# Performance work log

Measured on AMD Instinct MI355X. Metric: run time of the kernel, lower is better.

The kernel has to match this reference:

```python
import jax, jax.numpy as jnp
import numpy as np

N = 50000
E = 1280000
D = 64          # in_features = hidden_size = out_features
HEADS = 1
NEG_SLOPE = 0.2
EPS_COS = 1e-8
EPS_SM = 1e-16


def _xavier(key, shape):
    fan_in, fan_out = shape[0], shape[-1]
    lim = float(np.sqrt(6.0 / (fan_in + fan_out)))
    return jax.random.uniform(key, shape, jnp.float32, -lim, lim)


def setup_inputs() -> dict:
    key = jax.random.key(0)
    ks = jax.random.split(key, 16)
    x = jax.random.normal(ks[0], (N, D), jnp.float32)
    edge_index = jax.random.randint(ks[1], (2, E), 0, N, jnp.int64)
    edge_attr = jax.random.uniform(ks[2], (E,), jnp.float32)
    return {
        "x": x,
        "edge_index": edge_index,
        "edge_attr": edge_attr,
        # COSGAT layer 0 (in D -> out D, heads=1)
        "W0": _xavier(ks[3], (D, HEADS * D)),
        "att0": _xavier(ks[4], (HEADS, 2 * D)),
        "beta0": jnp.zeros((HEADS,), jnp.float32),
        "b0": jnp.zeros((HEADS * D,), jnp.float32),
        # COSGAT layer 1
        "W1": _xavier(ks[5], (D, HEADS * D)),
        "att1": _xavier(ks[6], (HEADS, 2 * D)),
        "beta1": jnp.zeros((HEADS,), jnp.float32),
        "b1": jnp.zeros((HEADS * D,), jnp.float32),
        # LinearEncoder residual branch
        "rW1": _xavier(ks[7], (D, D)),
        "rb1": jnp.zeros((D,), jnp.float32),
        "rW2": _xavier(ks[8], (D, D)),
        "rb2": jnp.zeros((D,), jnp.float32),
    }


def _seg_softmax(logits, idx, n):
    # softmax over edges grouped by target node idx; logits [E, H]
    m = jax.ops.segment_max(logits, idx, num_segments=n)
    ex = jnp.exp(logits - m[idx])
    s = jax.ops.segment_sum(ex, idx, num_segments=n)
    return ex / (s[idx] + EPS_SM)


def _cosgat(x, src, dst, w, W, att, beta, bias):
    n = x.shape[0]
    H = (x @ W).reshape(n, HEADS, -1)           # [N, H, C]
    Hi, Hj = H[dst], H[src]                      # [E, H, C]
    # GAT logits: att . [Hi || Hj]
    logits = (jnp.einsum('ehc,hc->eh', Hi, att[:, :H.shape[-1]])
              + jnp.einsum('ehc,hc->eh', Hj, att[:, H.shape[-1]:]))
    logits = jnp.where(logits >= 0, logits, NEG_SLOPE * logits)
    # cosine similarity on original features
    xi, xj = x[dst], x[src]
    ni = jnp.maximum(jnp.linalg.norm(xi, axis=-1), EPS_COS)
    nj = jnp.maximum(jnp.linalg.norm(xj, axis=-1), EPS_COS)
    cos = jnp.sum(xi * xj, axis=-1) / (ni * nj)  # [E]
    cos = jnp.broadcast_to(cos[:, None], logits.shape)
    gat_alpha = _seg_softmax(logits, dst, n)
    cos_alpha = _seg_softmax(cos, dst, n)
    b = jax.nn.sigmoid(beta)[None, :]            # [1, H]
    fused = (1.0 - b) * gat_alpha + b * cos_alpha
    w_cl = jnp.minimum(w, 4.0)
    gate = jnp.clip(1.0 - w_cl / 4.0, 0.0, 1.0)[:, None]  # [E, 1]
    final = _seg_softmax(fused * gate, dst, n)   # [E, H]
    msg = Hj * final[:, :, None]                 # [E, H, C]
    out = jax.ops.segment_sum(msg, dst, num_segments=n)
    out = out.reshape(n, -1) + bias              # concat heads + bias
    return jax.nn.elu(out)


def reference(x, edge_index, edge_attr, W0, att0, beta0, b0,
              W1, att1, beta1, b1, rW1, rb1, rW2, rb2):
    src, dst = edge_index[0], edge_index[1]      # PyG: i = target = edge_index[1]
    # residual MLP: Linear -> relu -> Linear (dropout p=0, eval)
    x_res = jax.nn.relu(x @ rW1 + rb1) @ rW2 + rb2
    h = _cosgat(x, src, dst, edge_attr, W0, att0, beta0, b0)
    h = jax.nn.elu(h)                            # inter-layer elu in encoder
    h = _cosgat(h, src, dst, edge_attr, W1, att1, beta1, b1)
    return h + x_res
```

## Files before the change

kernel.cpp:

```cpp
#include <hip/hip_runtime.h>
#include <hip/hip_bf16.h>
#include <math.h>


constexpr int D = 64;
constexpr int CAP = 64;
constexpr float NEG_SLOPE = 0.2f;
constexpr float EPS_COS = 1e-8f;
constexpr float EPS_SM = 1e-16f;

#if defined(__has_builtin)
#if __has_builtin(__builtin_amdgcn_cvt_pk_f32_fp8) && __has_builtin(__builtin_amdgcn_cvt_pk_fp8_f32)
#define HW_FP8 1
#endif
#endif

typedef float floatx2 __attribute__((ext_vector_type(2)));

__device__ __forceinline__ float wred_sum(float v) {
#pragma unroll
  for (int off = 32; off > 0; off >>= 1) v += __shfl_xor(v, off, 64);
  return v;
}
__device__ __forceinline__ float wred_max(float v) {
#pragma unroll
  for (int off = 32; off > 0; off >>= 1) v = fmaxf(v, __shfl_xor(v, off, 64));
  return v;
}
__device__ __forceinline__ float elu1(float x) { return x > 0.f ? x : __expf(x) - 1.f; }
__device__ __forceinline__ float sane(float v) {
  return (v == v && fabsf(v) < 1e30f) ? v : 0.f;
}
__device__ __forceinline__ float ldv(const void* p, size_t i, int f32) {
  return f32 ? ((const float*)p)[i]
             : __bfloat162float(((const __hip_bfloat16*)p)[i]);
}
__device__ __forceinline__ void stv(void* p, size_t i, int f32, float v) {
  if (f32) ((float*)p)[i] = v;
  else ((__hip_bfloat16*)p)[i] = __float2bfloat16(v);
}
__device__ __forceinline__ float b2f(unsigned short u) {
  return __uint_as_float(((unsigned int)u) << 16);
}
__device__ __forceinline__ void unp8(uint4 u, float* f) {
  f[0] = __uint_as_float(u.x << 16);
  f[1] = __uint_as_float(u.x & 0xffff0000u);
  f[2] = __uint_as_float(u.y << 16);
  f[3] = __uint_as_float(u.y & 0xffff0000u);
  f[4] = __uint_as_float(u.z << 16);
  f[5] = __uint_as_float(u.z & 0xffff0000u);
  f[6] = __uint_as_float(u.w << 16);
  f[7] = __uint_as_float(u.w & 0xffff0000u);
}

__device__ __forceinline__ unsigned char enc_fp8(float v) {
#ifdef HW_FP8
  int pk = __builtin_amdgcn_cvt_pk_fp8_f32(v, v, 0, false);
  return (unsigned char)(pk & 0xFF);
#else
  _Float16 h = (_Float16)v;
  unsigned short ub;
  __builtin_memcpy(&ub, &h, 2);
  return (unsigned char)((ub + 0x80) >> 8);
#endif
}
__device__ __forceinline__ void dec_fp8x8(uint2 u, float* f) {
#ifdef HW_FP8
  floatx2 a = __builtin_amdgcn_cvt_pk_f32_fp8(u.x, false);
  floatx2 b = __builtin_amdgcn_cvt_pk_f32_fp8(u.x, true);
  floatx2 c = __builtin_amdgcn_cvt_pk_f32_fp8(u.y, false);
  floatx2 d = __builtin_amdgcn_cvt_pk_f32_fp8(u.y, true);
  f[0] = a[0]; f[1] = a[1]; f[2] = b[0]; f[3] = b[1];
  f[4] = c[0]; f[5] = c[1]; f[6] = d[0]; f[7] = d[1];
#else
#pragma unroll
  for (int i = 0; i < 8; ++i) {
    unsigned int byte = (i < 4 ? (u.x >> (8 * i)) : (u.y >> (8 * (i - 4)))) & 0xFF;
    unsigned short hb = (unsigned short)(byte << 8);
    _Float16 h;
    __builtin_memcpy(&h, &hb, 2);
    f[i] = (float)h;
  }
#endif
}

__device__ __forceinline__ unsigned int pack_sg(int src, float g) {
  int gq = (int)(g * 16383.f + 0.5f);
  return ((unsigned int)src & 0x3FFFFu) | ((unsigned int)gq << 18);
}
__device__ __forceinline__ int upk_src(unsigned int e, int N) {
  return min((int)(e & 0x3FFFFu), N - 1);
}
__device__ __forceinline__ float upk_gate(unsigned int e) {
  return (float)(e >> 18) * (1.f / 16383.f);
}
__device__ __forceinline__ float gate_of(float w) {
  return fminf(fmaxf(1.f - 0.25f * fminf(w, 4.f), 0.f), 1.f);
}

__device__ float slow_cos(const unsigned char* __restrict__ fhat, int a, int b) {
  const uint2* fa = (const uint2*)(fhat + (size_t)a * D);
  const uint2* fb = (const uint2*)(fhat + (size_t)b * D);
  float dsum = 0.f;
  for (int q = 0; q < 8; ++q) {
    float va[8], vb[8];
    dec_fp8x8(fa[q], va);
    dec_fp8x8(fb[q], vb);
#pragma unroll
    for (int i = 0; i < 8; ++i) dsum += va[i] * vb[i];
  }
  return dsum;
}

__device__ __forceinline__ void prep_node(float f, int f32, int wid, int lane,
                                          const void* __restrict__ W,
                                          const void* __restrict__ att,
                                          unsigned char* __restrict__ fhat,
                                          __hip_bfloat16* __restrict__ Hmat,
                                          float* __restrict__ a_l,
                                          float* __restrict__ a_r,
                                          float* __restrict__ ls) {
  float n2 = wred_sum(f * f);
  float nrm = fmaxf(sqrtf(n2), EPS_COS);
  fhat[(size_t)wid * D + lane] = enc_fp8(f / nrm);
  ls[lane] = f;
  __syncthreads();
  float h0 = 0.f, h1 = 0.f, h2 = 0.f, h3 = 0.f;
  if (f32) {
    const float* Wf = (const float*)W;
#pragma unroll 4
    for (int k = 0; k < D; k += 4) {
      h0 += ls[k] * Wf[k * D + lane];
      h1 += ls[k + 1] * Wf[(k + 1) * D + lane];
      h2 += ls[k + 2] * Wf[(k + 2) * D + lane];
      h3 += ls[k + 3] * Wf[(k + 3) * D + lane];
    }
  } else {
    const __hip_bfloat16* Wb = (const __hip_bfloat16*)W;
#pragma unroll 4
    for (int k = 0; k < D; k += 4) {
      h0 += ls[k] * __bfloat162float(Wb[k * D + lane]);
      h1 += ls[k + 1] * __bfloat162float(Wb[(k + 1) * D + lane]);
      h2 += ls[k + 2] * __bfloat162float(Wb[(k + 2) * D + lane]);
      h3 += ls[k + 3] * __bfloat162float(Wb[(k + 3) * D + lane]);
    }
  }
  float Hc = (h0 + h1) + (h2 + h3);
  Hmat[(size_t)wid * D + lane] = __float2bfloat16(Hc);
  float al = wred_sum(Hc * ldv(att, lane, f32));
  float ar = wred_sum(Hc * ldv(att, D + lane, f32));
  if (lane == 0) {
    a_l[wid] = al;
    a_r[wid] = ar;
  }
  __syncthreads();
}

__global__ void __launch_bounds__(64) k_all(const unsigned short* __restrict__ xu,
                                            const int* __restrict__ ei,
                                            const void* __restrict__ w,
                                            int* __restrict__ flags,
                                            int* __restrict__ cnt,
                                            const void* __restrict__ x,
                                            const void* __restrict__ W,
                                            const void* __restrict__ att,
                                            unsigned char* __restrict__ fhat,
                                            __hip_bfloat16* __restrict__ Hmat,
                                            float* __restrict__ a_l,
                                            float* __restrict__ a_r,
                                            unsigned int* __restrict__ csr2,
                                            int N, int E) {
  __shared__ float ls[D];
  const int lane = threadIdx.x;
  const int b = blockIdx.x;
  float dv = b2f(xu[lane]);
  float da = fabsf(dv);
  unsigned long long m = __ballot(da > 1e-4f && da < 100.f);
  unsigned long long m2 = __ballot(ei[2 * lane + 1] != 0);
  const int f32 = (__popcll(m) >= 60) ? 0 : 1;
  const int wide = (m2 == 0ull) ? 1 : 0;
  if (b == 0 && lane == 0) {
    flags[0] = f32;
    flags[1] = wide;
  }
  const long long e0 = ((long long)b * E) / N;
  const long long e1 = ((long long)(b + 1) * E) / N;
  for (long long e = e0 + lane; e < e1; e += 64) {
    int ss, dd;
    if (wide) {
      ss = ei[2 * e];
      dd = ei[2 * (size_t)E + 2 * e];
    } else {
      ss = ei[e];
      dd = ei[(size_t)E + e];
    }
    float we = ldv(w, (size_t)e, f32);
    const int dc = min(max(dd, 0), N - 1);
    const int slot = atomicAdd(&cnt[dc], 1);
    if (slot < CAP)
      csr2[(size_t)dc * CAP + slot] = pack_sg(min(max(ss, 0), N - 1), gate_of(we));
  }
  if (b < N) {
    float f = ldv(x, (size_t)b * D + lane, f32);
    prep_node(f, f32, b, lane, W, att, fhat, Hmat, a_l, a_r, ls);
  }
}

__global__ void __launch_bounds__(64) k_prep(const void* __restrict__ xin,
                                             const void* __restrict__ W,
                                             const void* __restrict__ att,
                                             const int* __restrict__ flags,
                                             unsigned char* __restrict__ fhat,
                                             __hip_bfloat16* __restrict__ Hmat,
                                             float* __restrict__ a_l,
                                             float* __restrict__ a_r, int N) {
  __shared__ float ls[D];
  const int lane = threadIdx.x;
  const int wid = blockIdx.x;
  if (wid >= N) return;
  const int f32 = flags[0];
  float f = ldv(xin, (size_t)wid * D + lane, f32);
  prep_node(f, f32, wid, lane, W, att, fhat, Hmat, a_l, a_r, ls);
}

__global__ void __launch_bounds__(64, 8) k_edge(const int* __restrict__ cnt,
                                                const unsigned int* __restrict__ csr2,
                                                const int* __restrict__ ei,
                                                const void* __restrict__ w,
                                                const unsigned char* __restrict__ fhat,
                                                const __hip_bfloat16* __restrict__ Hmat,
                                                const float* __restrict__ a_l,
                                                const float* __restrict__ a_r,
                                                const void* __restrict__ beta,
                                                const void* __restrict__ bias,
                                                const void* __restrict__ x,
                                                const void* __restrict__ rW1,
                                                const void* __restrict__ rb1,
                                                const void* __restrict__ rW2,
                                                const void* __restrict__ rb2,
                                                const void* __restrict__ Wn,
                                                const void* __restrict__ attn,
                                                unsigned char* __restrict__ fh2,
                                                __hip_bfloat16* __restrict__ Hm2,
                                                float* __restrict__ al2,
                                                float* __restrict__ ar2,
                                                const int* __restrict__ flags,
                                                void* __restrict__ out,
                                                int N, int E, int mode) {
  const int lane = threadIdx.x;
  const int wid = blockIdx.x;
  __shared__ float2 lc[CAP];
  __shared__ float2 sg[CAP];
  __shared__ float lds_t[D];
  if (wid >= N) return;
  const int f32 = flags[0];
  const int g = lane >> 3;
  const int sub = lane & 7;
  const int degRaw = cnt[wid];
  const float aln = a_l[wid];
  const float bb = 1.f / (1.f + __expf(-ldv(beta, 0, f32)));
  const float ob = 1.f - bb;
  const char* HmatB = (const char*)Hmat;

  float v;
  if (degRaw <= CAP) {
    const int deg = degRaw;
    const int s = wid * CAP;
    float fn[8];
    dec_fp8x8(*(const uint2*)(fhat + (((unsigned)wid << 6) | ((unsigned)sub << 3))), fn);

    float m1 = -1e30f, m2 = -1e30f;
    uint4 hm[4];
#pragma unroll
    for (int kk = 0; kk < 4; ++kk) {
      const int base = kk * 8;
      if (base < deg) {
        const int j = base + g;
        const bool val = j < deg;
        const unsigned int en = val ? csr2[s + j] : (unsigned int)wid;
        const unsigned src = (unsigned)upk_src(en, N);
        float hv[8];
        dec_fp8x8(*(const uint2*)(fhat + ((src << 6) | ((unsigned)sub << 3))), hv);
        hm[kk] = *(const uint4*)(HmatB + ((src << 7) | ((unsigned)sub << 4)));
        float d = 0.f;
#pragma unroll
        for (int i = 0; i < 8; ++i) d += fn[i] * hv[i];
        d += __shfl_xor(d, 1, 64);
        d += __shfl_xor(d, 2, 64);
        d += __shfl_xor(d, 4, 64);
        float l = aln + a_r[src];
        l = (l >= 0.f) ? l : NEG_SLOPE * l;
        if (val) {
          m1 = fmaxf(m1, l);
          m2 = fmaxf(m2, d);
          if (sub == 0) lc[j] = make_float2(l, d);
        }
      }
    }
    for (int base = 32; base < deg; base += 8) {
      const int j = base + g;
      const bool val = j < deg;
      const unsigned int en = val ? csr2[s + j] : (unsigned int)wid;
      const unsigned src = (unsigned)upk_src(en, N);
      float hv[8];
      dec_fp8x8(*(const uint2*)(fhat + ((src << 6) | ((unsigned)sub << 3))), hv);
      float d = 0.f;
#pragma unroll
      for (int i = 0; i < 8; ++i) d += fn[i] * hv[i];
      d += __shfl_xor(d, 1, 64);
      d += __shfl_xor(d, 2, 64);
      d += __shfl_xor(d, 4, 64);
      float l = aln + a_r[src];
      l = (l >= 0.f) ? l : NEG_SLOPE * l;
      if (val) {
        m1 = fmaxf(m1, l);
        m2 = fmaxf(m2, d);
        if (sub == 0) lc[j] = make_float2(l, d);
      }
    }
    m1 = fmaxf(m1, __shfl_xor(m1, 8, 64));
    m1 = fmaxf(m1, __shfl_xor(m1, 16, 64));
    m1 = fmaxf(m1, __shfl_xor(m1, 32, 64));
    m2 = fmaxf(m2, __shfl_xor(m2, 8, 64));
    m2 = fmaxf(m2, __shfl_xor(m2, 16, 64));
    m2 = fmaxf(m2, __shfl_xor(m2, 32, 64));

    float el0 = 0.f, ec0 = 0.f, gg0 = 0.f;
    int q0 = 0;
    float ps1 = 0.f, ps2 = 0.f;
    if (lane < deg) {
      const unsigned int en = csr2[s + lane];
      q0 = upk_src(en, N);
      gg0 = upk_gate(en);
      float2 t = lc[lane];
      el0 = __expf(t.x - m1);
      ec0 = __expf(t.y - m2);
      ps1 = el0;
      ps2 = ec0;
    }
    const float rs1 = 1.f / (wred_sum(ps1) + EPS_SM);
    const float rs2 = 1.f / (wred_sum(ps2) + EPS_SM);

    float sp = 0.f;
    if (lane < deg) {
      float tt = (ob * el0 * rs1 + bb * ec0 * rs2) * gg0;
      float p0 = __expf(tt - 1.f);
      sp = p0;
      sg[lane] = make_float2(__int_as_float(q0), p0);
    }
    const float rinv = 1.f / (wred_sum(sp) + EPS_SM);

    float acc[8] = {0.f, 0.f, 0.f, 0.f, 0.f, 0.f, 0.f, 0.f};
#pragma unroll
    for (int kk = 0; kk < 4; ++kk) {
      const int base = kk * 8;
      if (base < deg) {
        const int j = base + g;
        const float pv = (j < deg) ? sg[j].y : 0.f;
        float hv[8];
        unp8(hm[kk], hv);
#pragma unroll
        for (int i = 0; i < 8; ++i) acc[i] += pv * hv[i];
      }
    }
    for (int base = 32; base < deg; base += 8) {
      const int j = base + g;
      float2 en = (j < deg) ? sg[j] : make_float2(__int_as_float(wid), 0.f);
      const float pv = en.y;
      const unsigned srcv = (unsigned)__float_as_int(en.x);
      float hv[8];
      unp8(*(const uint4*)(HmatB + ((srcv << 7) | ((unsigned)sub << 4))), hv);
#pragma unroll
      for (int i = 0; i < 8; ++i) acc[i] += pv * hv[i];
    }
#pragma unroll
    for (int i = 0; i < 8; ++i) {
      acc[i] += __shfl_xor(acc[i], 8, 64);
      acc[i] += __shfl_xor(acc[i], 16, 64);
      acc[i] += __shfl_xor(acc[i], 32, 64);
    }
    if (g == 0) {
#pragma unroll
      for (int i = 0; i < 8; ++i) lds_t[8 * sub + i] = acc[i];
    }
    v = lds_t[lane] * rinv + ldv(bias, lane, f32);
  } else {
    const int wide = flags[1];
    lds_t[lane] = 0.f;
    float m1 = -1e30f, m2 = -1e30f;
    for (int e64 = lane; e64 < E; e64 += 64) {
      int dd = wide ? ei[2 * (size_t)E + 2 * (size_t)e64] : ei[(size_t)E + e64];
      if (dd != wid) continue;
      int ss = wide ? ei[2 * (size_t)e64] : ei[e64];
      ss = min(max(ss, 0), N - 1);
      float l = aln + a_r[ss];
      l = (l >= 0.f) ? l : NEG_SLOPE * l;
      float c = slow_cos(fhat, wid, ss);
      m1 = fmaxf(m1, l);
      m2 = fmaxf(m2, c);
    }
    m1 = wred_max(m1);
    m2 = wred_max(m2);
    float ps1 = 0.f, ps2 = 0.f;
    for (int e64 = lane; e64 < E; e64 += 64) {
      int dd = wide ? ei[2 * (size_t)E + 2 * (size_t)e64] : ei[(size_t)E + e64];
      if (dd != wid) continue;
      int ss = wide ? ei[2 * (size_t)e64] : ei[e64];
      ss = min(max(ss, 0), N - 1);
      float l = aln + a_r[ss];
      l = (l >= 0.f) ? l : NEG_SLOPE * l;
      float c = slow_cos(fhat, wid, ss);
      ps1 += __expf(l - m1);
      ps2 += __expf(c - m2);
    }
    const float rs1 = 1.f / (wred_sum(ps1) + EPS_SM);
    const float rs2 = 1.f / (wred_sum(ps2) + EPS_SM);
    float sp = 0.f;
    for (int e64 = lane; e64 < E; e64 += 64) {
      int dd = wide ? ei[2 * (size_t)E + 2 * (size_t)e64] : ei[(size_t)E + e64];
      if (dd != wid) continue;
      int ss = wide ? ei[2 * (size_t)e64] : ei[e64];
      ss = min(max(ss, 0), N - 1);
      float l = aln + a_r[ss];
      l = (l >= 0.f) ? l : NEG_SLOPE * l;
      float c = slow_cos(fhat, wid, ss);
      float gx = gate_of(ldv(w, e64, f32));
      float px = __expf((ob * __expf(l - m1) * rs1 + bb * __expf(c - m2) * rs2) * gx - 1.f);
      sp += px;
      for (int q = 0; q < D; ++q)
        atomicAdd(&lds_t[q], px * __bfloat162float(Hmat[(size_t)ss * D + q]));
    }
    const float rinv = 1.f / (wred_sum(sp) + EPS_SM);
    v = lds_t[lane] * rinv + ldv(bias, lane, f32);
  }

  v = elu1(v);
  if (mode == 1) {
    float xv = ldv(x, (size_t)wid * D + lane, f32);
    float b0_ = ldv(rb1, lane, f32);
    __syncthreads();
    lds_t[lane] = xv;
    __syncthreads();
    float a2;
    float h0 = 0.f, h1 = 0.f, h2 = 0.f, h3 = 0.f;
    if (f32) {
      const float* w1 = (const float*)rW1;
      const float* w2 = (const float*)rW2;
#pragma unroll 4
      for (int k = 0; k < D; k += 4) {
        h0 += lds_t[k] * w1[k * D + lane];
        h1 += lds_t[k + 1] * w1[(k + 1) * D + lane];
        h2 += lds_t[k + 2] * w1[(k + 2) * D + lane];
        h3 += lds_t[k + 3] * w1[(k + 3) * D + lane];
      }
      float tr = fmaxf(b0_ + (h0 + h1) + (h2 + h3), 0.f);
      __syncthreads();
      lds_t[lane] = tr;
      __syncthreads();
      float g0 = 0.f, g1 = 0.f, g2 = 0.f, g3 = 0.f;
#pragma unroll 4
      for (int k = 0; k < D; k += 4) {
        g0 += lds_t[k] * w2[k * D + lane];
        g1 += lds_t[k + 1] * w2[(k + 1) * D + lane];
        g2 += lds_t[k + 2] * w2[(k + 2) * D + lane];
        g3 += lds_t[k + 3] * w2[(k + 3) * D + lane];
      }
      a2 = ((const float*)rb2)[lane] + (g0 + g1) + (g2 + g3);
    } else {
      const __hip_bfloat16* w1 = (const __hip_bfloat16*)rW1;
      const __hip_bfloat16* w2 = (const __hip_bfloat16*)rW2;
#pragma unroll 4
      for (int k = 0; k < D; k += 4) {
        h0 += lds_t[k] * __bfloat162float(w1[k * D + lane]);
        h1 += lds_t[k + 1] * __bfloat162float(w1[(k + 1) * D + lane]);
        h2 += lds_t[k + 2] * __bfloat162float(w1[(k + 2) * D + lane]);
        h3 += lds_t[k + 3] * __bfloat162float(w1[(k + 3) * D + lane]);
      }
      float tr = fmaxf(b0_ + (h0 + h1) + (h2 + h3), 0.f);
      __syncthreads();
      lds_t[lane] = tr;
      __syncthreads();
      float g0 = 0.f, g1 = 0.f, g2 = 0.f, g3 = 0.f;
#pragma unroll 4
      for (int k = 0; k < D; k += 4) {
        g0 += lds_t[k] * __bfloat162float(w2[k * D + lane]);
        g1 += lds_t[k + 1] * __bfloat162float(w2[(k + 1) * D + lane]);
        g2 += lds_t[k + 2] * __bfloat162float(w2[(k + 2) * D + lane]);
        g3 += lds_t[k + 3] * __bfloat162float(w2[(k + 3) * D + lane]);
      }
      a2 = __bfloat162float(((const __hip_bfloat16*)rb2)[lane]) + (g0 + g1) + (g2 + g3);
    }
    stv(out, (size_t)wid * D + lane, f32, sane(v + a2));
  } else {
    v = elu1(v);
    if (mode == 0) {
      __syncthreads();
      prep_node(sane(v), f32, wid, lane, Wn, attn, fh2, Hm2, al2, ar2, lds_t);
    } else {
      stv(out, (size_t)wid * D + lane, f32, sane(v));
    }
  }
}

extern "C" void kernel_launch(void* const* d_in, const int* in_sizes, int n_in,
                              void* d_out, int out_size, void* d_ws, size_t ws_size,
                              hipStream_t stream) {
  const void* x = d_in[0];
  const int* ei = (const int*)d_in[1];
  const void* w = d_in[2];
  const void* W0 = d_in[3];
  const void* att0 = d_in[4];
  const void* beta0 = d_in[5];
  const void* b0 = d_in[6];
  const void* W1 = d_in[7];
  const void* att1 = d_in[8];
  const void* beta1 = d_in[9];
  const void* b1 = d_in[10];
  const void* rW1 = d_in[11];
  const void* rb1 = d_in[12];
  const void* rW2 = d_in[13];
  const void* rb2 = d_in[14];

  const int N = in_sizes[0] / D;
  const int E = in_sizes[2];

  char* base = (char*)d_ws;
  size_t off = 0;
  auto alloc = [&](size_t bytes) -> void* {
    void* p = base + off;
    off += (bytes + 255) & ~(size_t)255;
    return p;
  };
  int* flags = (int*)alloc(256);
  int* cnt = (int*)alloc((size_t)N * 4);
  unsigned int* csr2 = (unsigned int*)alloc((size_t)N * CAP * 4);
  unsigned char* fhat = (unsigned char*)alloc((size_t)N * D);
  __hip_bfloat16* Hmat = (__hip_bfloat16*)alloc((size_t)N * D * 2);
  float* a_l = (float*)alloc((size_t)N * 4);
  float* a_r = (float*)alloc((size_t)N * 4);
  unsigned char* fhat2 = (unsigned char*)alloc((size_t)N * D);
  __hip_bfloat16* Hmat2 = (__hip_bfloat16*)alloc((size_t)N * D * 2);
  float* a_l2 = (float*)alloc((size_t)N * 4);
  float* a_r2 = (float*)alloc((size_t)N * 4);
  const bool fused = (off <= ws_size);

  hipMemsetAsync(cnt, 0, (size_t)N * 4, stream);
  k_all<<<N, 64, 0, stream>>>((const unsigned short*)x, ei, w, flags, cnt,
                              x, W0, att0, fhat, Hmat, a_l, a_r, csr2, N, E);

  if (fused) {
    k_edge<<<N, 64, 0, stream>>>(cnt, csr2, ei, w, fhat, Hmat, a_l, a_r,
                                 beta0, b0, x, rW1, rb1, rW2, rb2,
                                 W1, att1, fhat2, Hmat2, a_l2, a_r2,
                                 flags, d_out, N, E, 0);
    k_edge<<<N, 64, 0, stream>>>(cnt, csr2, ei, w, fhat2, Hmat2, a_l2, a_r2,
                                 beta1, b1, x, rW1, rb1, rW2, rb2,
                                 nullptr, nullptr, nullptr, nullptr, nullptr, nullptr,
                                 flags, d_out, N, E, 1);
  } else {
    k_edge<<<N, 64, 0, stream>>>(cnt, csr2, ei, w, fhat, Hmat, a_l, a_r,
                                 beta0, b0, x, rW1, rb1, rW2, rb2,
                                 nullptr, nullptr, nullptr, nullptr, nullptr, nullptr,
                                 flags, d_out, N, E, 2);
    k_prep<<<N, 64, 0, stream>>>(d_out, W1, att1, flags, fhat, Hmat, a_l, a_r, N);
    k_edge<<<N, 64, 0, stream>>>(cnt, csr2, ei, w, fhat, Hmat, a_l, a_r,
                                 beta1, b1, x, rW1, rb1, rW2, rb2,
                                 nullptr, nullptr, nullptr, nullptr, nullptr, nullptr,
                                 flags, d_out, N, E, 1);
  }
}
```

Before: 321.1 us.

## Split binning into wide edge kernel and add register-resident weight prep kernels

Edge binning moves out of the per-node fused kernel into its own 256-thread kernel that loads two edges per thread with vector loads. Node preparation and the residual MLP become persistent grid-stride kernels that keep the weight columns in registers, so W is not re-read for every node. The residual MLP is precomputed into a float buffer and added in the final edge pass. The two-layer fused path is replaced by a sequence of separate prep and edge launches, which needs extra workspace (hbuf, xres) and adds launches and intermediate memory traffic.

```diff
diff --git a/kernel.cpp b/kernel.cpp
--- a/kernel.cpp
+++ b/kernel.cpp
@@ -156,53 +156,175 @@
   __syncthreads();
 }
 
-__global__ void __launch_bounds__(64) k_all(const unsigned short* __restrict__ xu,
-                                            const int* __restrict__ ei,
-                                            const void* __restrict__ w,
-                                            int* __restrict__ flags,
-                                            int* __restrict__ cnt,
-                                            const void* __restrict__ x,
-                                            const void* __restrict__ W,
-                                            const void* __restrict__ att,
-                                            unsigned char* __restrict__ fhat,
-                                            __hip_bfloat16* __restrict__ Hmat,
-                                            float* __restrict__ a_l,
-                                            float* __restrict__ a_r,
-                                            unsigned int* __restrict__ csr2,
-                                            int N, int E) {
+__global__ void __launch_bounds__(256) k_bin(const unsigned short* __restrict__ xu,
+                                             const int* __restrict__ ei,
+                                             const void* __restrict__ w,
+                                             int* __restrict__ flags,
+                                             int* __restrict__ cnt,
+                                             unsigned int* __restrict__ csr2,
+                                             int N, int E) {
+  __shared__ int sf[2];
+  const int tid = threadIdx.x;
+  if (tid < 64) {
+    float v = b2f(xu[tid]);
+    float a = fabsf(v);
+    unsigned long long m = __ballot(a > 1e-4f && a < 100.f);
+    unsigned long long m2 = __ballot(ei[2 * tid + 1] != 0);
+    if (tid == 0) {
+      sf[0] = (__popcll(m) >= 60) ? 0 : 1;
+      sf[1] = (m2 == 0ull) ? 1 : 0;
+      if (blockIdx.x == 0) {
+        flags[0] = sf[0];
+        flags[1] = sf[1];
+      }
+    }
+  }
+  __syncthreads();
+  const int f32 = sf[0], wide = sf[1];
+  const int e0 = (blockIdx.x * 256 + tid) * 2;
+  if (e0 >= E) return;
+  const bool has1 = (e0 + 1 < E);
+  int s0, s1, d0, d1;
+  if (wide) {
+    int4 vs = *(const int4*)(ei + 2 * (size_t)e0);
+    int4 vd = *(const int4*)(ei + 2 * (size_t)E + 2 * (size_t)e0);
+    s0 = vs.x; s1 = vs.z; d0 = vd.x; d1 = vd.z;
+  } else {
+    int2 vs = *(const int2*)(ei + e0);
+    int2 vd = *(const int2*)(ei + (size_t)E + e0);
+    s0 = vs.x; s1 = vs.y; d0 = vd.x; d1 = vd.y;
+  }
+  float w0, w1 = 0.f;
+  if (f32) {
+    float2 wv = *(const float2*)((const float*)w + e0);
+    w0 = wv.x; w1 = wv.y;
+  } else {
+    const __hip_bfloat16* wb = (const __hip_bfloat16*)w;
+    w0 = __bfloat162float(wb[e0]);
+    if (has1) w1 = __bfloat162float(wb[e0 + 1]);
+  }
+  int d0c = min(max(d0, 0), N - 1);
+  int slot0 = atomicAdd(&cnt[d0c], 1);
+  if (slot0 < CAP)
+    csr2[(size_t)d0c * CAP + slot0] = pack_sg(min(max(s0, 0), N - 1), gate_of(w0));
+  if (has1) {
+    int d1c = min(max(d1, 0), N - 1);
+    int slot1 = atomicAdd(&cnt[d1c], 1);
+    if (slot1 < CAP)
+      csr2[(size_t)d1c * CAP + slot1] = pack_sg(min(max(s1, 0), N - 1), gate_of(w1));
+  }
+}
+
+__global__ void __launch_bounds__(64, 4) k_prepW(const void* __restrict__ xin,
+                                                 const void* __restrict__ W,
+                                                 const void* __restrict__ att,
+                                                 const int* __restrict__ flags,
+                                                 unsigned char* __restrict__ fhat,
+                                                 __hip_bfloat16* __restrict__ Hmat,
+                                                 float* __restrict__ a_l,
+                                                 float* __restrict__ a_r, int N) {
   __shared__ float ls[D];
   const int lane = threadIdx.x;
-  const int b = blockIdx.x;
-  float dv = b2f(xu[lane]);
-  float da = fabsf(dv);
-  unsigned long long m = __ballot(da > 1e-4f && da < 100.f);
-  unsigned long long m2 = __ballot(ei[2 * lane + 1] != 0);
-  const int f32 = (__popcll(m) >= 60) ? 0 : 1;
-  const int wide = (m2 == 0ull) ? 1 : 0;
-  if (b == 0 && lane == 0) {
-    flags[0] = f32;
-    flags[1] = wide;
-  }
-  const long long e0 = ((long long)b * E) / N;
-  const long long e1 = ((long long)(b + 1) * E) / N;
-  for (long long e = e0 + lane; e < e1; e += 64) {
-    int ss, dd;
-    if (wide) {
-      ss = ei[2 * e];
-      dd = ei[2 * (size_t)E + 2 * e];
-    } else {
-      ss = ei[e];
-      dd = ei[(size_t)E + e];
-    }
-    float we = ldv(w, (size_t)e, f32);
-    const int dc = min(max(dd, 0), N - 1);
-    const int slot = atomicAdd(&cnt[dc], 1);
-    if (slot < CAP)
-      csr2[(size_t)dc * CAP + slot] = pack_sg(min(max(ss, 0), N - 1), gate_of(we));
-  }
-  if (b < N) {
-    float f = ldv(x, (size_t)b * D + lane, f32);
-    prep_node(f, f32, b, lane, W, att, fhat, Hmat, a_l, a_r, ls);
+  const int f32 = flags[0];
+  float wreg[D];
+  if (f32) {
+    const float* Wf = (const float*)W;
+#pragma unroll
+    for (int k = 0; k < D; ++k) wreg[k] = Wf[k * D + lane];
+  } else {
+    const __hip_bfloat16* Wb = (const __hip_bfloat16*)W;
+#pragma unroll
+    for (int k = 0; k < D; ++k) wreg[k] = __bfloat162float(Wb[k * D + lane]);
+  }
+  const float attl = ldv(att, lane, f32);
+  const float attr = ldv(att, D + lane, f32);
+  float f = (blockIdx.x < (unsigned)N) ? ldv(xin, (size_t)blockIdx.x * D + lane, f32) : 0.f;
+  for (int wid = blockIdx.x; wid < N; wid += gridDim.x) {
+    const int nwid = wid + gridDim.x;
+    float fnx = (nwid < N) ? ldv(xin, (size_t)nwid * D + lane, f32) : 0.f;
+    float n2 = wred_sum(f * f);
+    float nrm = fmaxf(sqrtf(n2), EPS_COS);
+    fhat[(size_t)wid * D + lane] = enc_fp8(f / nrm);
+    ls[lane] = f;
+    __syncthreads();
+    float h0 = 0.f, h1 = 0.f, h2 = 0.f, h3 = 0.f;
+#pragma unroll
+    for (int k = 0; k < D; k += 4) {
+      h0 += ls[k] * wreg[k];
+      h1 += ls[k + 1] * wreg[k + 1];
+      h2 += ls[k + 2] * wreg[k + 2];
+      h3 += ls[k + 3] * wreg[k + 3];
+    }
+    float Hc = (h0 + h1) + (h2 + h3);
+    Hmat[(size_t)wid * D + lane] = __float2bfloat16(Hc);
+    float al = wred_sum(Hc * attl);
+    float ar = wred_sum(Hc * attr);
+    if (lane == 0) {
+      a_l[wid] = al;
+      a_r[wid] = ar;
+    }
+    __syncthreads();
+    f = fnx;
+  }
+}
+
+__global__ void __launch_bounds__(64, 3) k_resW(const void* __restrict__ xin,
+                                                const void* __restrict__ rW1,
+                                                const void* __restrict__ rb1,
+                                                const void* __restrict__ rW2,
+                                                const void* __restrict__ rb2,
+                                                const int* __restrict__ flags,
+                                                float* __restrict__ xres, int N) {
+  __shared__ float ls[D];
+  const int lane = threadIdx.x;
+  const int f32 = flags[0];
+  float w1reg[D], w2reg[D];
+  if (f32) {
+    const float* w1 = (const float*)rW1;
+    const float* w2 = (const float*)rW2;
+#pragma unroll
+    for (int k = 0; k < D; ++k) w1reg[k] = w1[k * D + lane];
+#pragma unroll
+    for (int k = 0; k < D; ++k) w2reg[k] = w2[k * D + lane];
+  } else {
+    const __hip_bfloat16* w1 = (const __hip_bfloat16*)rW1;
+    const __hip_bfloat16* w2 = (const __hip_bfloat16*)rW2;
+#pragma unroll
+    for (int k = 0; k < D; ++k) w1reg[k] = __bfloat162float(w1[k * D + lane]);
+#pragma unroll
+    for (int k = 0; k < D; ++k) w2reg[k] = __bfloat162float(w2[k * D + lane]);
+  }
+  const float b1v = ldv(rb1, lane, f32);
+  const float b2v = ldv(rb2, lane, f32);
+  float f = (blockIdx.x < (unsigned)N) ? ldv(xin, (size_t)blockIdx.x * D + lane, f32) : 0.f;
+  for (int wid = blockIdx.x; wid < N; wid += gridDim.x) {
+    const int nwid = wid + gridDim.x;
+    float fnx = (nwid < N) ? ldv(xin, (size_t)nwid * D + lane, f32) : 0.f;
+    ls[lane] = f;
+    __syncthreads();
+    float h0 = b1v, h1 = 0.f, h2 = 0.f, h3 = 0.f;
+#pragma unroll
+    for (int k = 0; k < D; k += 4) {
+      h0 += ls[k] * w1reg[k];
+      h1 += ls[k + 1] * w1reg[k + 1];
+      h2 += ls[k + 2] * w1reg[k + 2];
+      h3 += ls[k + 3] * w1reg[k + 3];
+    }
+    float tr = fmaxf((h0 + h1) + (h2 + h3), 0.f);
+    __syncthreads();
+    ls[lane] = tr;
+    __syncthreads();
+    float g0 = b2v, g1 = 0.f, g2 = 0.f, g3 = 0.f;
+#pragma unroll
+    for (int k = 0; k < D; k += 4) {
+      g0 += ls[k] * w2reg[k];
+      g1 += ls[k + 1] * w2reg[k + 1];
+      g2 += ls[k + 2] * w2reg[k + 2];
+      g3 += ls[k + 3] * w2reg[k + 3];
+    }
+    xres[(size_t)wid * D + lane] = (g0 + g1) + (g2 + g3);
+    __syncthreads();
+    f = fnx;
   }
 }
 
@@ -244,6 +366,7 @@
                                                 __hip_bfloat16* __restrict__ Hm2,
                                                 float* __restrict__ al2,
                                                 float* __restrict__ ar2,
+                                                const float* __restrict__ xres,
                                                 const int* __restrict__ flags,
                                                 void* __restrict__ out,
                                                 int N, int E, int mode) {
@@ -435,7 +558,10 @@
   }
 
   v = elu1(v);
-  if (mode == 1) {
+  if (mode == 3) {
+    float a2 = xres[(size_t)wid * D + lane];
+    stv(out, (size_t)wid * D + lane, f32, sane(v + a2));
+  } else if (mode == 1) {
     float xv = ldv(x, (size_t)wid * D + lane, f32);
     float b0_ = ldv(rb1, lane, f32);
     __syncthreads();
@@ -538,34 +664,55 @@
   __hip_bfloat16* Hmat = (__hip_bfloat16*)alloc((size_t)N * D * 2);
   float* a_l = (float*)alloc((size_t)N * 4);
   float* a_r = (float*)alloc((size_t)N * 4);
+  const size_t common_off = off;
+  float* hbuf = (float*)alloc((size_t)N * D * 4);
+  float* xres = (float*)alloc((size_t)N * D * 4);
+  const bool tierA = (off <= ws_size);
+  off = common_off;
   unsigned char* fhat2 = (unsigned char*)alloc((size_t)N * D);
   __hip_bfloat16* Hmat2 = (__hip_bfloat16*)alloc((size_t)N * D * 2);
   float* a_l2 = (float*)alloc((size_t)N * 4);
   float* a_r2 = (float*)alloc((size_t)N * 4);
-  const bool fused = (off <= ws_size);
+  const bool tierB = (off <= ws_size);
+
+  const int eb2 = (E / 2 + 255) / 256;
 
   hipMemsetAsync(cnt, 0, (size_t)N * 4, stream);
-  k_all<<<N, 64, 0, stream>>>((const unsigned short*)x, ei, w, flags, cnt,
-                              x, W0, att0, fhat, Hmat, a_l, a_r, csr2, N, E);
-
-  if (fused) {
+  k_bin<<<eb2, 256, 0, stream>>>((const unsigned short*)x, ei, w, flags, cnt,
+                                 csr2, N, E);
+
+  if (tierA) {
+    k_prepW<<<4096, 64, 0, stream>>>(x, W0, att0, flags, fhat, Hmat, a_l, a_r, N);
+    k_resW<<<3072, 64, 0, stream>>>(x, rW1, rb1, rW2, rb2, flags, xres, N);
+    k_edge<<<N, 64, 0, stream>>>(cnt, csr2, ei, w, fhat, Hmat, a_l, a_r,
+                                 beta0, b0, x, rW1, rb1, rW2, rb2,
+                                 nullptr, nullptr, nullptr, nullptr, nullptr, nullptr,
+                                 nullptr, flags, hbuf, N, E, 2);
+    k_prepW<<<4096, 64, 0, stream>>>(hbuf, W1, att1, flags, fhat, Hmat, a_l, a_r, N);
+    k_edge<<<N, 64, 0, stream>>>(cnt, csr2, ei, w, fhat, Hmat, a_l, a_r,
+                                 beta1, b1, x, rW1, rb1, rW2, rb2,
+                                 nullptr, nullptr, nullptr, nullptr, nullptr, nullptr,
+                                 xres, flags, d_out, N, E, 3);
+  } else if (tierB) {
+    k_prep<<<N, 64, 0, stream>>>(x, W0, att0, flags, fhat, Hmat, a_l, a_r, N);
     k_edge<<<N, 64, 0, stream>>>(cnt, csr2, ei, w, fhat, Hmat, a_l, a_r,
                                  beta0, b0, x, rW1, rb1, rW2, rb2,
                                  W1, att1, fhat2, Hmat2, a_l2, a_r2,
-                                 flags, d_out, N, E, 0);
+                                 nullptr, flags, d_out, N, E, 0);
     k_edge<<<N, 64, 0, stream>>>(cnt, csr2, ei, w, fhat2, Hmat2, a_l2, a_r2,
                                  beta1, b1, x, rW1, rb1, rW2, rb2,
                                  nullptr, nullptr, nullptr, nullptr, nullptr, nullptr,
-                                 flags, d_out, N, E, 1);
+                                 nullptr, flags, d_out, N, E, 1);
   } else {
+    k_prep<<<N, 64, 0, stream>>>(x, W0, att0, flags, fhat, Hmat, a_l, a_r, N);
     k_edge<<<N, 64, 0, stream>>>(cnt, csr2, ei, w, fhat, Hmat, a_l, a_r,
                                  beta0, b0, x, rW1, rb1, rW2, rb2,
                                  nullptr, nullptr, nullptr, nullptr, nullptr, nullptr,
-                                 flags, d_out, N, E, 2);
+                                 nullptr, flags, d_out, N, E, 2);
     k_prep<<<N, 64, 0, stream>>>(d_out, W1, att1, flags, fhat, Hmat, a_l, a_r, N);
     k_edge<<<N, 64, 0, stream>>>(cnt, csr2, ei, w, fhat, Hmat, a_l, a_r,
                                  beta1, b1, x, rW1, rb1, rW2, rb2,
                                  nullptr, nullptr, nullptr, nullptr, nullptr, nullptr,
-                                 flags, d_out, N, E, 1);
-  }
-}
+                                 nullptr, flags, d_out, N, E, 1);
+  }
+}
```

Result: slower. 366.3 us (+14.1%).
